# Kernel optimization log

Measured on AMD Instinct MI355X. Metric: run time of the kernel, lower is better.

The kernel has to match this reference:

```python
import jax, jax.numpy as jnp
import numpy as np

WS = 7          # window size
NH = 8          # num heads
EMBED = 512
HD = EMBED // NH


def _rel_pos_index(ws):
    coords = np.stack(np.meshgrid(np.arange(ws), np.arange(ws), indexing='ij'))  # [2,ws,ws]
    flat = coords.reshape(2, -1)                                                 # [2, ws*ws]
    rel = flat[:, :, None] - flat[:, None, :]                                    # [2, L, L]
    rel = rel.transpose(1, 2, 0).astype(np.int32)                                # [L, L, 2]
    rel[..., 0] += ws - 1
    rel[..., 1] += ws - 1
    rel[..., 0] *= 2 * ws - 1
    return rel.sum(-1)                                                           # [L, L]


def setup_inputs() -> dict:
    key = jax.random.key(0)
    ks = jax.random.split(key, 6)
    B, H, W, C = 8, 126, 126, EMBED
    s = 1.0 / np.sqrt(C)
    return {
        'x': jax.random.normal(ks[0], (B, H * W, C), jnp.float32),
        'in_proj_weight': jax.random.normal(ks[1], (3 * C, C), jnp.float32) * s,
        'in_proj_bias': jax.random.normal(ks[2], (3 * C,), jnp.float32) * 0.02,
        'out_proj_weight': jax.random.normal(ks[3], (C, C), jnp.float32) * s,
        'out_proj_bias': jnp.zeros((C,), jnp.float32),
        'rpe_table': jax.random.normal(ks[4], ((2 * WS - 1) ** 2, NH), jnp.float32) * 0.02,
        'rel_index': jnp.asarray(_rel_pos_index(WS)),
        'H': H,
        'W': W,
    }


def _window_permute(x, ws):
    # x: [B, H, W, C] -> [ws*ws, B*qh*qw, C]  (ISA local permute)
    B, H, W, C = x.shape
    qh, qw = H // ws, W // ws
    x = x.reshape(B, qh, ws, qw, ws, C)
    x = jnp.transpose(x, (2, 4, 0, 1, 3, 5))          # ph, pw, B, qh, qw, C
    return x.reshape(ws * ws, B * qh * qw, C)


def _window_unpermute(x, ws, B, H, W):
    qh, qw = H // ws, W // ws
    C = x.shape[-1]
    x = x.reshape(ws, ws, B, qh, qw, C)
    x = jnp.transpose(x, (2, 3, 0, 4, 1, 5))          # B, qh, ph, qw, pw, C
    return x.reshape(B, H, W, C)


def reference(x, in_proj_weight, in_proj_bias, out_proj_weight, out_proj_bias,
              rpe_table, rel_index, H, W):
    B, N, C = x.shape
    xh = x.reshape(B, H, W, C)
    # H, W divisible by window size -> pad/depad are identity
    xp = _window_permute(xh, WS)                       # [L, Bw, C], L = WS*WS
    L, Bw, _ = xp.shape

    qkv = xp @ in_proj_weight.T + in_proj_bias         # [L, Bw, 3C]
    q, k, v = jnp.split(qkv, 3, axis=-1)
    q = q.reshape(L, Bw, NH, HD) * (HD ** -0.5)
    k = k.reshape(L, Bw, NH, HD)
    v = v.reshape(L, Bw, NH, HD)

    scores = jnp.einsum('lbhd,mbhd->bhlm', q, k)       # [Bw, NH, L, L]
    rpe = rpe_table[rel_index]                          # [L, L, NH]
    scores = scores + jnp.transpose(rpe, (2, 0, 1))[None]
    attn = jax.nn.softmax(scores, axis=-1)
    out = jnp.einsum('bhlm,mbhd->lbhd', attn, v).reshape(L, Bw, C)
    out = out @ out_proj_weight.T + out_proj_bias       # [L, Bw, C]

    out = _window_unpermute(out, WS, B, H, W)
    return out.reshape(B, N, C)
```

## Files before the change

### kernel.cpp

```cpp
#include <hip/hip_runtime.h>
#include <hip/hip_bf16.h>
#include <stdint.h>

typedef __attribute__((ext_vector_type(8))) short short8;
typedef __attribute__((ext_vector_type(4))) float f32x4;
typedef __hip_bfloat16 bf16;

#define MFMA16(a, b, c) __builtin_amdgcn_mfma_f32_16x16x32_bf16(a, b, c, 0, 0, 0)

__device__ __forceinline__ uint32_t swz(uint32_t row, uint32_t bir) {
  return bir ^ ((row & 7u) << 4);
}
__device__ __forceinline__ short f2bs(float v) {
  bf16 b = __float2bfloat16(v);
  return *reinterpret_cast<short*>(&b);
}
__device__ __forceinline__ float b2f(bf16 b) { return __bfloat162float(b); }

__device__ __forceinline__ short8 cvt8(f32x4 a, f32x4 b) {
  short8 v;
  v[0] = f2bs(a[0]); v[1] = f2bs(a[1]); v[2] = f2bs(a[2]); v[3] = f2bs(a[3]);
  v[4] = f2bs(b[0]); v[5] = f2bs(b[1]); v[6] = f2bs(b[2]); v[7] = f2bs(b[3]);
  return v;
}

__device__ __forceinline__ void gl_lds16(const void* g, void* l) {
  __builtin_amdgcn_global_load_lds(
      (const __attribute__((address_space(1))) unsigned int*)g,
      (__attribute__((address_space(3))) unsigned int*)l, 16, 0, 0);
}

__global__ __launch_bounds__(256) void k_conv_w4(
    const float* __restrict__ wqkv, const float* __restrict__ bqkv,
    const float* __restrict__ wo,   const float* __restrict__ bo,
    const float* __restrict__ rpe,  const int* __restrict__ relidx,
    char* __restrict__ wqkvb, bf16* __restrict__ bqkvb,
    char* __restrict__ wob,   bf16* __restrict__ bob,
    bf16* __restrict__ rpew)
{
  int b = blockIdx.x, t = threadIdx.x;
  if (b < 384) {
    long i = (long)b * 2048 + t * 8;
    int row = (int)(i >> 9);
    uint32_t g = ((uint32_t)i & 511u) >> 3;
    f32x4 a = *(const f32x4*)(wqkv + i), c = *(const f32x4*)(wqkv + i + 4);
    *reinterpret_cast<short8*>(wqkvb + (size_t)row * 1024 + ((g * 16) ^ ((row & 7u) << 4))) = cvt8(a, c);
  } else if (b < 512) {
    long i = (long)(b - 384) * 2048 + t * 8;
    int row = (int)(i >> 9);
    uint32_t g = ((uint32_t)i & 511u) >> 3;
    f32x4 a = *(const f32x4*)(wo + i), c = *(const f32x4*)(wo + i + 4);
    *reinterpret_cast<short8*>(wob + (size_t)row * 1024 + ((g * 16) ^ ((row & 7u) << 4))) = cvt8(a, c);
  } else if (b == 512) {
    for (int j = t; j < 1536; j += 256) bqkvb[j] = __float2bfloat16(bqkv[j]);
    for (int j = t; j < 512;  j += 256) bob[j]  = __float2bfloat16(bo[j]);
  } else {
    int h = b - 513;
    for (int e = t; e < 3136; e += 256) {
      int q = e >> 6, c = e & 63;
      float v = (c < 49) ? rpe[(long)relidx[q * 49 + c] * 8 + h] : 0.f;
      rpew[h * 3136 + e] = __float2bfloat16(v);
    }
  }
}

__global__ __launch_bounds__(256) void k_conv_x3(
    const float* __restrict__ x, char* __restrict__ xb)
{
  int R  = blockIdx.x * 4 + (threadIdx.x >> 6);
  int c8 = threadIdx.x & 63;
  f32x4 a = {0.f, 0.f, 0.f, 0.f}, b = a;
  if (R < 127008) {
    a = *(const f32x4*)(x + (size_t)R * 512 + c8 * 8);
    b = *(const f32x4*)(x + (size_t)R * 512 + c8 * 8 + 4);
  }
  *reinterpret_cast<short8*>(xb + (size_t)R * 1024 + ((uint32_t)(c8 * 16) ^ ((R & 7u) << 4))) = cvt8(a, b);
}

__global__ __launch_bounds__(256) void k_qkv_gemm6(
    const char* __restrict__ xb,
    const char* __restrict__ wqkvb,
    const bf16* __restrict__ bqkvb,
    char* __restrict__ blob,
    int cb_)
{
  __shared__ __align__(16) char sA[16384];
  __shared__ __align__(16) char sB[16384];

  const int tid = threadIdx.x, lane = tid & 63, w = tid >> 6;
  const int r16 = lane & 15, hi = lane >> 4;

  const int raw = blockIdx.x;
  const int xcd = raw & 7, grp = raw >> 3;
  const int nb = grp % 12, mg = grp / 12;
  const int mtile = mg * 8 + xcd;
  if (mtile >= 249) return;
  const int row0 = cb_ * 31752 + mtile * 128;

  const char* Abase = xb + (size_t)row0 * 1024;
  const char* Bbase = wqkvb + (size_t)nb * 131072;

  const uint32_t rxA = ((uint32_t)((r16 + row0) & 7)) << 4;
  const uint32_t rxB = ((uint32_t)(r16 & 7)) << 4;

  const f32x4 fz = {0.f, 0.f, 0.f, 0.f};
  f32x4 acc[4][4];
  #pragma unroll
  for (int m = 0; m < 4; ++m)
    #pragma unroll
    for (int n = 0; n < 4; ++n) acc[m][n] = fz;

  for (int k0 = 0; k0 < 8; ++k0) {
    if (k0) __syncthreads();
    #pragma unroll
    for (int j = 0; j < 8; ++j) {
      int ch = w * 8 + j;
      if (ch < 16)
        gl_lds16(Abase + (size_t)(ch * 8 + (lane >> 3)) * 1024 + k0 * 128 + (lane & 7) * 16,
                 sA + ch * 1024);
      else {
        int c2 = ch - 16;
        gl_lds16(Bbase + (size_t)(c2 * 8 + (lane >> 3)) * 1024 + k0 * 128 + (lane & 7) * 16,
                 sB + c2 * 1024);
      }
    }
    __syncthreads();

    #pragma unroll
    for (int ks = 0; ks < 2; ++ks) {
      uint32_t cb = (uint32_t)((ks * 4 + hi) * 16);
      short8 aF[4], bF[4];
      #pragma unroll
      for (int m = 0; m < 4; ++m)
        aF[m] = *(const short8*)(sA + ((w & 1) * 64 + m * 16 + r16) * 128 + (cb ^ rxA));
      #pragma unroll
      for (int n = 0; n < 4; ++n)
        bF[n] = *(const short8*)(sB + ((w >> 1) * 64 + n * 16 + r16) * 128 + (cb ^ rxB));
      #pragma unroll
      for (int m = 0; m < 4; ++m)
        #pragma unroll
        for (int n = 0; n < 4; ++n)
          acc[m][n] = MFMA16(aF[m], bF[n], acc[m][n]);
    }
  }

  const int gcol = nb * 128 + (w >> 1) * 64;
  const int t = gcol >> 9;
  const int h = (gcol >> 6) & 7;
  const float scale = (t == 0) ? 0.125f : 1.0f;

  float bias4[4];
  #pragma unroll
  for (int n = 0; n < 4; ++n) bias4[n] = b2f(bqkvb[gcol + n * 16 + r16]);

  #pragma unroll
  for (int m = 0; m < 4; ++m)
    #pragma unroll
    for (int r = 0; r < 4; ++r) {
      int rnat = row0 + (w & 1) * 64 + m * 16 + hi * 4 + r;
      int rem = rnat - cb_ * 31752;
      if (rem >= 31752) continue;
      int b2 = rem / 15876, rem2 = rem - b2 * 15876;
      int y = rem2 / 126, xc = rem2 - y * 126;
      int qi = y / 7, ph = y - qi * 7;
      int qj = xc / 7, pw = xc - qj * 7;
      int wiL = b2 * 324 + qi * 18 + qj, wrow = ph * 7 + pw;
      char* tile = blob + ((size_t)(t * 648 + wiL) * 8 + h) * 8192;
      #pragma unroll
      for (int n = 0; n < 4; ++n) {
        int d = n * 16 + r16;
        bf16 v = __float2bfloat16((acc[m][n][r] + bias4[n]) * scale);
        if (t < 2)
          *(bf16*)(tile + wrow * 128 + ((uint32_t)(2 * d) ^ ((wrow & 7u) << 4))) = v;
        else
          *(bf16*)(tile + wrow * 128 + 2 * d) = v;
      }
    }
}

__global__ __launch_bounds__(256) void k_attn6(
    const char* __restrict__ blob,
    const bf16* __restrict__ rpew,
    char* __restrict__ attnb,
    int cb_)
{
  __shared__ __align__(16) char sQ[8192];
  __shared__ __align__(16) char sK[8192];
  __shared__ __align__(16) char sV[8192];
  __shared__ __align__(16) char sP[8192];

  const int tid = threadIdx.x, lane = tid & 63, w = tid >> 6;
  const int r16 = lane & 15, hi = lane >> 4;
  const int wiL = blockIdx.x >> 3, h = blockIdx.x & 7;

  const char* qb = blob + ((size_t)(0 * 648 + wiL) * 8 + h) * 8192;
  const char* kb = blob + ((size_t)(1 * 648 + wiL) * 8 + h) * 8192;
  const char* vb = blob + ((size_t)(2 * 648 + wiL) * 8 + h) * 8192;

  #pragma unroll
  for (int j = 0; j < 6; ++j) {
    int ch = w * 6 + j;
    int rg = ch >> 3, sub = ch & 7;
    const char* src = (rg == 0 ? qb : rg == 1 ? kb : vb) + sub * 1024 + lane * 16;
    char* dst = (rg == 0 ? sQ : rg == 1 ? sK : sV) + sub * 1024;
    gl_lds16(src, dst);
  }
  __syncthreads();

  const f32x4 fz = {0.f, 0.f, 0.f, 0.f};

  f32x4 s[4];
  #pragma unroll
  for (int n = 0; n < 4; ++n) s[n] = fz;
  #pragma unroll
  for (int k0 = 0; k0 < 2; ++k0) {
    int qrow = w * 16 + r16;
    short8 a = *(const short8*)(sQ + qrow * 128 + swz(qrow, k0 * 64 + hi * 16));
    #pragma unroll
    for (int n = 0; n < 4; ++n) {
      int krow = n * 16 + r16;
      short8 kf = *(const short8*)(sK + krow * 128 + swz(krow, k0 * 64 + hi * 16));
      s[n] = MFMA16(a, kf, s[n]);
    }
  }

  #pragma unroll
  for (int n = 0; n < 4; ++n) {
    int col = n * 16 + r16;
    #pragma unroll
    for (int rr = 0; rr < 4; ++rr) {
      int qrow = w * 16 + hi * 4 + rr;
      int qc = qrow < 49 ? qrow : 48;
      float sv = s[n][rr] + b2f(rpew[h * 3136 + qc * 64 + col]);
      if (col >= 49) sv = -1e30f;
      s[n][rr] = sv;
    }
  }
  #pragma unroll
  for (int rr = 0; rr < 4; ++rr) {
    float mx = fmaxf(fmaxf(s[0][rr], s[1][rr]), fmaxf(s[2][rr], s[3][rr]));
    mx = fmaxf(mx, __shfl_xor(mx, 1));
    mx = fmaxf(mx, __shfl_xor(mx, 2));
    mx = fmaxf(mx, __shfl_xor(mx, 4));
    mx = fmaxf(mx, __shfl_xor(mx, 8));
    float su = 0.f;
    #pragma unroll
    for (int n = 0; n < 4; ++n) {
      float e = __expf(s[n][rr] - mx);
      s[n][rr] = e;
      su += e;
    }
    su += __shfl_xor(su, 1);
    su += __shfl_xor(su, 2);
    su += __shfl_xor(su, 4);
    su += __shfl_xor(su, 8);
    float inv = 1.f / su;
    #pragma unroll
    for (int n = 0; n < 4; ++n) s[n][rr] *= inv;
  }

  char* pw = sP + w * 2048;
  #pragma unroll
  for (int n = 0; n < 4; ++n)
    #pragma unroll
    for (int rr = 0; rr < 4; ++rr) {
      int rl = hi * 4 + rr, col = n * 16 + r16;
      *(bf16*)(pw + rl * 128 + swz(rl, 2 * col)) = __float2bfloat16(s[n][rr]);
    }
  __syncthreads();

  char* sVt = sQ;
  {
    int k = tid >> 2, c0 = (tid & 3) * 16;
    short8 v0 = *(const short8*)(sV + k * 128 + 2 * c0);
    short8 v1 = *(const short8*)(sV + k * 128 + 2 * c0 + 16);
    #pragma unroll
    for (int e = 0; e < 8; ++e) {
      int c = c0 + e;
      *(short*)(sVt + c * 128 + ((uint32_t)(2 * k) ^ ((c & 7u) << 4))) = v0[e];
      int c2 = c0 + 8 + e;
      *(short*)(sVt + c2 * 128 + ((uint32_t)(2 * k) ^ ((c2 & 7u) << 4))) = v1[e];
    }
  }
  __syncthreads();

  f32x4 o[4];
  #pragma unroll
  for (int n = 0; n < 4; ++n) o[n] = fz;
  #pragma unroll
  for (int k0 = 0; k0 < 2; ++k0) {
    short8 a = *(const short8*)(pw + r16 * 128 + swz(r16, k0 * 64 + hi * 16));
    #pragma unroll
    for (int n = 0; n < 4; ++n) {
      int d = n * 16 + r16;
      short8 vf = *(const short8*)(sVt + d * 128 + swz(d, k0 * 64 + hi * 16));
      o[n] = MFMA16(a, vf, o[n]);
    }
  }

  const int b2 = wiL / 324, wr = wiL - b2 * 324;
  const int qi = wr / 18, qj = wr - qi * 18;
  const int rowBase = (cb_ * 2 + b2) * 15876 + qi * 882 + qj * 7;
  #pragma unroll
  for (int n = 0; n < 4; ++n) {
    int d = n * 16 + r16;
    #pragma unroll
    for (int r = 0; r < 4; ++r) {
      int wrow = w * 16 + hi * 4 + r;
      if (wrow < 49) {
        int rnat = rowBase + (wrow / 7) * 126 + wrow % 7;
        *(bf16*)(attnb + (size_t)rnat * 1024 +
                 ((uint32_t)(h * 128 + 2 * d) ^ ((rnat & 7u) << 4))) =
            __float2bfloat16(o[n][r]);
      }
    }
  }
}

__global__ __launch_bounds__(256) void k_out_gemm3(
    const char* __restrict__ attnb,
    const char* __restrict__ wob,
    const bf16* __restrict__ bob,
    float* __restrict__ out)
{
  __shared__ __align__(16) char sA[16384];
  __shared__ __align__(16) char sB[16384];

  const int tid = threadIdx.x, lane = tid & 63, w = tid >> 6;
  const int r16 = lane & 15, hi = lane >> 4;

  const int raw = blockIdx.x;
  const int xcd = raw & 7, grp = raw >> 3;
  const int nb = grp & 3, mg = grp >> 2;
  const int mtile = mg * 8 + xcd;
  if (mtile >= 993) return;
  const int row0 = mtile * 128;

  const char* Abase = attnb + (size_t)row0 * 1024;
  const char* Bbase = wob + (size_t)nb * 131072;

  const f32x4 fz = {0.f, 0.f, 0.f, 0.f};
  f32x4 acc[4][4];
  #pragma unroll
  for (int m = 0; m < 4; ++m)
    #pragma unroll
    for (int n = 0; n < 4; ++n) acc[m][n] = fz;

  for (int k0 = 0; k0 < 8; ++k0) {
    if (k0) __syncthreads();
    #pragma unroll
    for (int j = 0; j < 8; ++j) {
      int ch = w * 8 + j;
      if (ch < 16)
        gl_lds16(Abase + (size_t)(ch * 8 + (lane >> 3)) * 1024 + k0 * 128 + (lane & 7) * 16,
                 sA + ch * 1024);
      else {
        int c2 = ch - 16;
        gl_lds16(Bbase + (size_t)(c2 * 8 + (lane >> 3)) * 1024 + k0 * 128 + (lane & 7) * 16,
                 sB + c2 * 1024);
      }
    }
    __syncthreads();

    #pragma unroll
    for (int ks = 0; ks < 2; ++ks) {
      uint32_t cb = (uint32_t)((ks * 4 + hi) * 16) ^ ((r16 & 7u) << 4);
      short8 aF[4], bF[4];
      #pragma unroll
      for (int m = 0; m < 4; ++m)
        aF[m] = *(const short8*)(sA + ((w & 1) * 64 + m * 16 + r16) * 128 + cb);
      #pragma unroll
      for (int n = 0; n < 4; ++n)
        bF[n] = *(const short8*)(sB + ((w >> 1) * 64 + n * 16 + r16) * 128 + cb);
      #pragma unroll
      for (int m = 0; m < 4; ++m)
        #pragma unroll
        for (int n = 0; n < 4; ++n)
          acc[m][n] = MFMA16(aF[m], bF[n], acc[m][n]);
    }
  }

  #pragma unroll
  for (int n = 0; n < 4; ++n) {
    int col = nb * 128 + (w >> 1) * 64 + n * 16 + r16;
    float bias = b2f(bob[col]);
    #pragma unroll
    for (int m = 0; m < 4; ++m)
      #pragma unroll
      for (int r = 0; r < 4; ++r) {
        int row = row0 + (w & 1) * 64 + m * 16 + hi * 4 + r;
        if (row < 127008)
          out[(size_t)row * 512 + col] = acc[m][n][r] + bias;
      }
  }
}

extern "C" void kernel_launch(void* const* d_in, const int* in_sizes, int n_in,
                              void* d_out, int out_size, void* d_ws, size_t ws_size,
                              hipStream_t stream) {
  const float* x      = (const float*)d_in[0];
  const float* wqkv   = (const float*)d_in[1];
  const float* bqkv   = (const float*)d_in[2];
  const float* wo     = (const float*)d_in[3];
  const float* bo     = (const float*)d_in[4];
  const float* rpe    = (const float*)d_in[5];
  const int*   relidx = (const int*)d_in[6];

  char* ws = (char*)d_ws;
  const size_t OFF_XB    = 256;
  const size_t SZ_XB     = 127232ull * 1024;
  const size_t OFF_ATTNB = OFF_XB + SZ_XB;
  const size_t SZ_ATTNB  = 127104ull * 1024;
  const size_t OFF_BLOB  = OFF_ATTNB + SZ_ATTNB;
  const size_t SZ_BLOB   = 3ull * 648 * 8 * 8192;
  const size_t OFF_WQKV  = OFF_BLOB + SZ_BLOB;
  const size_t OFF_WO    = OFF_WQKV + 1536ull * 1024;
  const size_t OFF_BQKV  = OFF_WO + 512ull * 1024;
  const size_t OFF_BO    = OFF_BQKV + 3072;
  const size_t OFF_RPEW  = OFF_BO + 1024;

  char* xb    = ws + OFF_XB;
  char* attnb = ws + OFF_ATTNB;
  char* blob  = ws + OFF_BLOB;
  char* wqkvb = ws + OFF_WQKV;
  char* wob   = ws + OFF_WO;
  bf16* bqkvb = (bf16*)(ws + OFF_BQKV);
  bf16* bob   = (bf16*)(ws + OFF_BO);
  bf16* rpew  = (bf16*)(ws + OFF_RPEW);

  k_conv_w4<<<dim3(521), dim3(256), 0, stream>>>(wqkv, bqkv, wo, bo, rpe, relidx,
                                                 wqkvb, bqkvb, wob, bob, rpew);
  k_conv_x3<<<dim3(31808), dim3(256), 0, stream>>>(x, xb);
  for (int c = 0; c < 4; ++c) {
    k_qkv_gemm6<<<dim3(3072), dim3(256), 0, stream>>>(xb, wqkvb, bqkvb, blob, c);
    k_attn6<<<dim3(5184), dim3(256), 0, stream>>>(blob, rpew, attnb, c);
  }
  k_out_gemm3<<<dim3(4000), dim3(256), 0, stream>>>(attnb, wob, bob, (float*)d_out);
}
```

Measured before the change: 704.5 us.

## Fuse fp32-to-bf16 conversion of x into the QKV GEMM A-tile load

Removes the standalone x conversion kernel and the bf16 staging buffer. The QKV GEMM now loads fp32 rows of x into registers, prefetches the next K-slice, converts to bf16 and writes swizzled into LDS, while B tiles still use direct global-to-LDS loads. This avoids the extra write and reread of the converted buffer, but each N-block now reads fp32 activations at twice the bytes and converts them redundantly across the 12 column blocks.

```diff
diff --git a/kernel.cpp b/kernel.cpp
--- a/kernel.cpp
+++ b/kernel.cpp
@@ -64,21 +64,8 @@
   }
 }
 
-__global__ __launch_bounds__(256) void k_conv_x3(
-    const float* __restrict__ x, char* __restrict__ xb)
-{
-  int R  = blockIdx.x * 4 + (threadIdx.x >> 6);
-  int c8 = threadIdx.x & 63;
-  f32x4 a = {0.f, 0.f, 0.f, 0.f}, b = a;
-  if (R < 127008) {
-    a = *(const f32x4*)(x + (size_t)R * 512 + c8 * 8);
-    b = *(const f32x4*)(x + (size_t)R * 512 + c8 * 8 + 4);
-  }
-  *reinterpret_cast<short8*>(xb + (size_t)R * 1024 + ((uint32_t)(c8 * 16) ^ ((R & 7u) << 4))) = cvt8(a, b);
-}
-
-__global__ __launch_bounds__(256) void k_qkv_gemm6(
-    const char* __restrict__ xb,
+__global__ __launch_bounds__(256) void k_qkv_gemm7(
+    const float* __restrict__ x,
     const char* __restrict__ wqkvb,
     const bf16* __restrict__ bqkvb,
     char* __restrict__ blob,
@@ -97,11 +84,257 @@
   if (mtile >= 249) return;
   const int row0 = cb_ * 31752 + mtile * 128;
 
-  const char* Abase = xb + (size_t)row0 * 1024;
+  const int lrow  = tid >> 1;
+  const int halfc = tid & 1;
+  const int growc = (row0 + lrow < 127008) ? row0 + lrow : 127007;
+  const float* xrow = x + (size_t)growc * 512 + halfc * 32;
+  char* sArow = sA + lrow * 128;
+  const uint32_t wkey = ((uint32_t)(lrow & 7)) << 4;
+
   const char* Bbase = wqkvb + (size_t)nb * 131072;
-
-  const uint32_t rxA = ((uint32_t)((r16 + row0) & 7)) << 4;
-  const uint32_t rxB = ((uint32_t)(r16 & 7)) << 4;
+  const uint32_t rxL = ((uint32_t)(r16 & 7)) << 4;
+
+  const f32x4 fz = {0.f, 0.f, 0.f, 0.f};
+  f32x4 acc[4][4];
+  #pragma unroll
+  for (int m = 0; m < 4; ++m)
+    #pragma unroll
+    for (int n = 0; n < 4; ++n) acc[m][n] = fz;
+
+  f32x4 pa[8];
+  #pragma unroll
+  for (int j = 0; j < 8; ++j) pa[j] = *(const f32x4*)(xrow + j * 4);
+
+  for (int k0 = 0; k0 < 8; ++k0) {
+    if (k0) __syncthreads();
+    #pragma unroll
+    for (int j = 0; j < 4; ++j)
+      *(short8*)(sArow + (((uint32_t)(halfc * 64 + j * 16)) ^ wkey)) =
+          cvt8(pa[2 * j], pa[2 * j + 1]);
+    #pragma unroll
+    for (int j = 0; j < 4; ++j) {
+      int ch = w * 4 + j;
+      gl_lds16(Bbase + (size_t)(ch * 8 + (lane >> 3)) * 1024 + k0 * 128 + (lane & 7) * 16,
+               sB + ch * 1024);
+    }
+    __syncthreads();
+    if (k0 < 7) {
+      const float* src = xrow + (k0 + 1) * 64;
+      #pragma unroll
+      for (int j = 0; j < 8; ++j) pa[j] = *(const f32x4*)(src + j * 4);
+    }
+    #pragma unroll
+    for (int ks = 0; ks < 2; ++ks) {
+      uint32_t cb = (uint32_t)((ks * 4 + hi) * 16);
+      short8 aF[4], bF[4];
+      #pragma unroll
+      for (int m = 0; m < 4; ++m)
+        aF[m] = *(const short8*)(sA + ((w & 1) * 64 + m * 16 + r16) * 128 + (cb ^ rxL));
+      #pragma unroll
+      for (int n = 0; n < 4; ++n)
+        bF[n] = *(const short8*)(sB + ((w >> 1) * 64 + n * 16 + r16) * 128 + (cb ^ rxL));
+      #pragma unroll
+      for (int m = 0; m < 4; ++m)
+        #pragma unroll
+        for (int n = 0; n < 4; ++n)
+          acc[m][n] = MFMA16(aF[m], bF[n], acc[m][n]);
+    }
+  }
+
+  const int gcol = nb * 128 + (w >> 1) * 64;
+  const int t = gcol >> 9;
+  const int h = (gcol >> 6) & 7;
+  const float scale = (t == 0) ? 0.125f : 1.0f;
+
+  float bias4[4];
+  #pragma unroll
+  for (int n = 0; n < 4; ++n) bias4[n] = b2f(bqkvb[gcol + n * 16 + r16]);
+
+  #pragma unroll
+  for (int m = 0; m < 4; ++m)
+    #pragma unroll
+    for (int r = 0; r < 4; ++r) {
+      int rnat = row0 + (w & 1) * 64 + m * 16 + hi * 4 + r;
+      int rem = rnat - cb_ * 31752;
+      if (rem >= 31752) continue;
+      int b2 = rem / 15876, rem2 = rem - b2 * 15876;
+      int y = rem2 / 126, xc = rem2 - y * 126;
+      int qi = y / 7, ph = y - qi * 7;
+      int qj = xc / 7, pw = xc - qj * 7;
+      int wiL = b2 * 324 + qi * 18 + qj, wrow = ph * 7 + pw;
+      char* tile = blob + ((size_t)(t * 648 + wiL) * 8 + h) * 8192;
+      #pragma unroll
+      for (int n = 0; n < 4; ++n) {
+        int d = n * 16 + r16;
+        bf16 v = __float2bfloat16((acc[m][n][r] + bias4[n]) * scale);
+        if (t < 2)
+          *(bf16*)(tile + wrow * 128 + ((uint32_t)(2 * d) ^ ((wrow & 7u) << 4))) = v;
+        else
+          *(bf16*)(tile + wrow * 128 + 2 * d) = v;
+      }
+    }
+}
+
+__global__ __launch_bounds__(256) void k_attn6(
+    const char* __restrict__ blob,
+    const bf16* __restrict__ rpew,
+    char* __restrict__ attnb,
+    int cb_)
+{
+  __shared__ __align__(16) char sQ[8192];
+  __shared__ __align__(16) char sK[8192];
+  __shared__ __align__(16) char sV[8192];
+  __shared__ __align__(16) char sP[8192];
+
+  const int tid = threadIdx.x, lane = tid & 63, w = tid >> 6;
+  const int r16 = lane & 15, hi = lane >> 4;
+  const int wiL = blockIdx.x >> 3, h = blockIdx.x & 7;
+
+  const char* qb = blob + ((size_t)(0 * 648 + wiL) * 8 + h) * 8192;
+  const char* kb = blob + ((size_t)(1 * 648 + wiL) * 8 + h) * 8192;
+  const char* vb = blob + ((size_t)(2 * 648 + wiL) * 8 + h) * 8192;
+
+  #pragma unroll
+  for (int j = 0; j < 6; ++j) {
+    int ch = w * 6 + j;
+    int rg = ch >> 3, sub = ch & 7;
+    const char* src = (rg == 0 ? qb : rg == 1 ? kb : vb) + sub * 1024 + lane * 16;
+    char* dst = (rg == 0 ? sQ : rg == 1 ? sK : sV) + sub * 1024;
+    gl_lds16(src, dst);
+  }
+  __syncthreads();
+
+  const f32x4 fz = {0.f, 0.f, 0.f, 0.f};
+
+  f32x4 s[4];
+  #pragma unroll
+  for (int n = 0; n < 4; ++n) s[n] = fz;
+  #pragma unroll
+  for (int k0 = 0; k0 < 2; ++k0) {
+    int qrow = w * 16 + r16;
+    short8 a = *(const short8*)(sQ + qrow * 128 + swz(qrow, k0 * 64 + hi * 16));
+    #pragma unroll
+    for (int n = 0; n < 4; ++n) {
+      int krow = n * 16 + r16;
+      short8 kf = *(const short8*)(sK + krow * 128 + swz(krow, k0 * 64 + hi * 16));
+      s[n] = MFMA16(a, kf, s[n]);
+    }
+  }
+
+  #pragma unroll
+  for (int n = 0; n < 4; ++n) {
+    int col = n * 16 + r16;
+    #pragma unroll
+    for (int rr = 0; rr < 4; ++rr) {
+      int qrow = w * 16 + hi * 4 + rr;
+      int qc = qrow < 49 ? qrow : 48;
+      float sv = s[n][rr] + b2f(rpew[h * 3136 + qc * 64 + col]);
+      if (col >= 49) sv = -1e30f;
+      s[n][rr] = sv;
+    }
+  }
+  #pragma unroll
+  for (int rr = 0; rr < 4; ++rr) {
+    float mx = fmaxf(fmaxf(s[0][rr], s[1][rr]), fmaxf(s[2][rr], s[3][rr]));
+    mx = fmaxf(mx, __shfl_xor(mx, 1));
+    mx = fmaxf(mx, __shfl_xor(mx, 2));
+    mx = fmaxf(mx, __shfl_xor(mx, 4));
+    mx = fmaxf(mx, __shfl_xor(mx, 8));
+    float su = 0.f;
+    #pragma unroll
+    for (int n = 0; n < 4; ++n) {
+      float e = __expf(s[n][rr] - mx);
+      s[n][rr] = e;
+      su += e;
+    }
+    su += __shfl_xor(su, 1);
+    su += __shfl_xor(su, 2);
+    su += __shfl_xor(su, 4);
+    su += __shfl_xor(su, 8);
+    float inv = 1.f / su;
+    #pragma unroll
+    for (int n = 0; n < 4; ++n) s[n][rr] *= inv;
+  }
+
+  char* pw = sP + w * 2048;
+  #pragma unroll
+  for (int n = 0; n < 4; ++n)
+    #pragma unroll
+    for (int rr = 0; rr < 4; ++rr) {
+      int rl = hi * 4 + rr, col = n * 16 + r16;
+      *(bf16*)(pw + rl * 128 + swz(rl, 2 * col)) = __float2bfloat16(s[n][rr]);
+    }
+  __syncthreads();
+
+  char* sVt = sQ;
+  {
+    int k = tid >> 2, c0 = (tid & 3) * 16;
+    short8 v0 = *(const short8*)(sV + k * 128 + 2 * c0);
+    short8 v1 = *(const short8*)(sV + k * 128 + 2 * c0 + 16);
+    #pragma unroll
+    for (int e = 0; e < 8; ++e) {
+      int c = c0 + e;
+      *(short*)(sVt + c * 128 + ((uint32_t)(2 * k) ^ ((c & 7u) << 4))) = v0[e];
+      int c2 = c0 + 8 + e;
+      *(short*)(sVt + c2 * 128 + ((uint32_t)(2 * k) ^ ((c2 & 7u) << 4))) = v1[e];
+    }
+  }
+  __syncthreads();
+
+  f32x4 o[4];
+  #pragma unroll
+  for (int n = 0; n < 4; ++n) o[n] = fz;
+  #pragma unroll
+  for (int k0 = 0; k0 < 2; ++k0) {
+    short8 a = *(const short8*)(pw + r16 * 128 + swz(r16, k0 * 64 + hi * 16));
+    #pragma unroll
+    for (int n = 0; n < 4; ++n) {
+      int d = n * 16 + r16;
+      short8 vf = *(const short8*)(sVt + d * 128 + swz(d, k0 * 64 + hi * 16));
+      o[n] = MFMA16(a, vf, o[n]);
+    }
+  }
+
+  const int b2 = wiL / 324, wr = wiL - b2 * 324;
+  const int qi = wr / 18, qj = wr - qi * 18;
+  const int rowBase = (cb_ * 2 + b2) * 15876 + qi * 882 + qj * 7;
+  #pragma unroll
+  for (int n = 0; n < 4; ++n) {
+    int d = n * 16 + r16;
+    #pragma unroll
+    for (int r = 0; r < 4; ++r) {
+      int wrow = w * 16 + hi * 4 + r;
+      if (wrow < 49) {
+        int rnat = rowBase + (wrow / 7) * 126 + wrow % 7;
+        *(bf16*)(attnb + (size_t)rnat * 1024 +
+                 ((uint32_t)(h * 128 + 2 * d) ^ ((rnat & 7u) << 4))) =
+            __float2bfloat16(o[n][r]);
+      }
+    }
+  }
+}
+
+__global__ __launch_bounds__(256) void k_out_gemm3(
+    const char* __restrict__ attnb,
+    const char* __restrict__ wob,
+    const bf16* __restrict__ bob,
+    float* __restrict__ out)
+{
+  __shared__ __align__(16) char sA[16384];
+  __shared__ __align__(16) char sB[16384];
+
+  const int tid = threadIdx.x, lane = tid & 63, w = tid >> 6;
+  const int r16 = lane & 15, hi = lane >> 4;
+
+  const int raw = blockIdx.x;
+  const int xcd = raw & 7, grp = raw >> 3;
+  const int nb = grp & 3, mg = grp >> 2;
+  const int mtile = mg * 8 + xcd;
+  if (mtile >= 993) return;
+  const int row0 = mtile * 128;
+
+  const char* Abase = attnb + (size_t)row0 * 1024;
+  const char* Bbase = wob + (size_t)nb * 131072;
 
   const f32x4 fz = {0.f, 0.f, 0.f, 0.f};
   f32x4 acc[4][4];
@@ -128,242 +361,6 @@
 
     #pragma unroll
     for (int ks = 0; ks < 2; ++ks) {
-      uint32_t cb = (uint32_t)((ks * 4 + hi) * 16);
-      short8 aF[4], bF[4];
-      #pragma unroll
-      for (int m = 0; m < 4; ++m)
-        aF[m] = *(const short8*)(sA + ((w & 1) * 64 + m * 16 + r16) * 128 + (cb ^ rxA));
-      #pragma unroll
-      for (int n = 0; n < 4; ++n)
-        bF[n] = *(const short8*)(sB + ((w >> 1) * 64 + n * 16 + r16) * 128 + (cb ^ rxB));
-      #pragma unroll
-      for (int m = 0; m < 4; ++m)
-        #pragma unroll
-        for (int n = 0; n < 4; ++n)
-          acc[m][n] = MFMA16(aF[m], bF[n], acc[m][n]);
-    }
-  }
-
-  const int gcol = nb * 128 + (w >> 1) * 64;
-  const int t = gcol >> 9;
-  const int h = (gcol >> 6) & 7;
-  const float scale = (t == 0) ? 0.125f : 1.0f;
-
-  float bias4[4];
-  #pragma unroll
-  for (int n = 0; n < 4; ++n) bias4[n] = b2f(bqkvb[gcol + n * 16 + r16]);
-
-  #pragma unroll
-  for (int m = 0; m < 4; ++m)
-    #pragma unroll
-    for (int r = 0; r < 4; ++r) {
-      int rnat = row0 + (w & 1) * 64 + m * 16 + hi * 4 + r;
-      int rem = rnat - cb_ * 31752;
-      if (rem >= 31752) continue;
-      int b2 = rem / 15876, rem2 = rem - b2 * 15876;
-      int y = rem2 / 126, xc = rem2 - y * 126;
-      int qi = y / 7, ph = y - qi * 7;
-      int qj = xc / 7, pw = xc - qj * 7;
-      int wiL = b2 * 324 + qi * 18 + qj, wrow = ph * 7 + pw;
-      char* tile = blob + ((size_t)(t * 648 + wiL) * 8 + h) * 8192;
-      #pragma unroll
-      for (int n = 0; n < 4; ++n) {
-        int d = n * 16 + r16;
-        bf16 v = __float2bfloat16((acc[m][n][r] + bias4[n]) * scale);
-        if (t < 2)
-          *(bf16*)(tile + wrow * 128 + ((uint32_t)(2 * d) ^ ((wrow & 7u) << 4))) = v;
-        else
-          *(bf16*)(tile + wrow * 128 + 2 * d) = v;
-      }
-    }
-}
-
-__global__ __launch_bounds__(256) void k_attn6(
-    const char* __restrict__ blob,
-    const bf16* __restrict__ rpew,
-    char* __restrict__ attnb,
-    int cb_)
-{
-  __shared__ __align__(16) char sQ[8192];
-  __shared__ __align__(16) char sK[8192];
-  __shared__ __align__(16) char sV[8192];
-  __shared__ __align__(16) char sP[8192];
-
-  const int tid = threadIdx.x, lane = tid & 63, w = tid >> 6;
-  const int r16 = lane & 15, hi = lane >> 4;
-  const int wiL = blockIdx.x >> 3, h = blockIdx.x & 7;
-
-  const char* qb = blob + ((size_t)(0 * 648 + wiL) * 8 + h) * 8192;
-  const char* kb = blob + ((size_t)(1 * 648 + wiL) * 8 + h) * 8192;
-  const char* vb = blob + ((size_t)(2 * 648 + wiL) * 8 + h) * 8192;
-
-  #pragma unroll
-  for (int j = 0; j < 6; ++j) {
-    int ch = w * 6 + j;
-    int rg = ch >> 3, sub = ch & 7;
-    const char* src = (rg == 0 ? qb : rg == 1 ? kb : vb) + sub * 1024 + lane * 16;
-    char* dst = (rg == 0 ? sQ : rg == 1 ? sK : sV) + sub * 1024;
-    gl_lds16(src, dst);
-  }
-  __syncthreads();
-
-  const f32x4 fz = {0.f, 0.f, 0.f, 0.f};
-
-  f32x4 s[4];
-  #pragma unroll
-  for (int n = 0; n < 4; ++n) s[n] = fz;
-  #pragma unroll
-  for (int k0 = 0; k0 < 2; ++k0) {
-    int qrow = w * 16 + r16;
-    short8 a = *(const short8*)(sQ + qrow * 128 + swz(qrow, k0 * 64 + hi * 16));
-    #pragma unroll
-    for (int n = 0; n < 4; ++n) {
-      int krow = n * 16 + r16;
-      short8 kf = *(const short8*)(sK + krow * 128 + swz(krow, k0 * 64 + hi * 16));
-      s[n] = MFMA16(a, kf, s[n]);
-    }
-  }
-
-  #pragma unroll
-  for (int n = 0; n < 4; ++n) {
-    int col = n * 16 + r16;
-    #pragma unroll
-    for (int rr = 0; rr < 4; ++rr) {
-      int qrow = w * 16 + hi * 4 + rr;
-      int qc = qrow < 49 ? qrow : 48;
-      float sv = s[n][rr] + b2f(rpew[h * 3136 + qc * 64 + col]);
-      if (col >= 49) sv = -1e30f;
-      s[n][rr] = sv;
-    }
-  }
-  #pragma unroll
-  for (int rr = 0; rr < 4; ++rr) {
-    float mx = fmaxf(fmaxf(s[0][rr], s[1][rr]), fmaxf(s[2][rr], s[3][rr]));
-    mx = fmaxf(mx, __shfl_xor(mx, 1));
-    mx = fmaxf(mx, __shfl_xor(mx, 2));
-    mx = fmaxf(mx, __shfl_xor(mx, 4));
-    mx = fmaxf(mx, __shfl_xor(mx, 8));
-    float su = 0.f;
-    #pragma unroll
-    for (int n = 0; n < 4; ++n) {
-      float e = __expf(s[n][rr] - mx);
-      s[n][rr] = e;
-      su += e;
-    }
-    su += __shfl_xor(su, 1);
-    su += __shfl_xor(su, 2);
-    su += __shfl_xor(su, 4);
-    su += __shfl_xor(su, 8);
-    float inv = 1.f / su;
-    #pragma unroll
-    for (int n = 0; n < 4; ++n) s[n][rr] *= inv;
-  }
-
-  char* pw = sP + w * 2048;
-  #pragma unroll
-  for (int n = 0; n < 4; ++n)
-    #pragma unroll
-    for (int rr = 0; rr < 4; ++rr) {
-      int rl = hi * 4 + rr, col = n * 16 + r16;
-      *(bf16*)(pw + rl * 128 + swz(rl, 2 * col)) = __float2bfloat16(s[n][rr]);
-    }
-  __syncthreads();
-
-  char* sVt = sQ;
-  {
-    int k = tid >> 2, c0 = (tid & 3) * 16;
-    short8 v0 = *(const short8*)(sV + k * 128 + 2 * c0);
-    short8 v1 = *(const short8*)(sV + k * 128 + 2 * c0 + 16);
-    #pragma unroll
-    for (int e = 0; e < 8; ++e) {
-      int c = c0 + e;
-      *(short*)(sVt + c * 128 + ((uint32_t)(2 * k) ^ ((c & 7u) << 4))) = v0[e];
-      int c2 = c0 + 8 + e;
-      *(short*)(sVt + c2 * 128 + ((uint32_t)(2 * k) ^ ((c2 & 7u) << 4))) = v1[e];
-    }
-  }
-  __syncthreads();
-
-  f32x4 o[4];
-  #pragma unroll
-  for (int n = 0; n < 4; ++n) o[n] = fz;
-  #pragma unroll
-  for (int k0 = 0; k0 < 2; ++k0) {
-    short8 a = *(const short8*)(pw + r16 * 128 + swz(r16, k0 * 64 + hi * 16));
-    #pragma unroll
-    for (int n = 0; n < 4; ++n) {
-      int d = n * 16 + r16;
-      short8 vf = *(const short8*)(sVt + d * 128 + swz(d, k0 * 64 + hi * 16));
-      o[n] = MFMA16(a, vf, o[n]);
-    }
-  }
-
-  const int b2 = wiL / 324, wr = wiL - b2 * 324;
-  const int qi = wr / 18, qj = wr - qi * 18;
-  const int rowBase = (cb_ * 2 + b2) * 15876 + qi * 882 + qj * 7;
-  #pragma unroll
-  for (int n = 0; n < 4; ++n) {
-    int d = n * 16 + r16;
-    #pragma unroll
-    for (int r = 0; r < 4; ++r) {
-      int wrow = w * 16 + hi * 4 + r;
-      if (wrow < 49) {
-        int rnat = rowBase + (wrow / 7) * 126 + wrow % 7;
-        *(bf16*)(attnb + (size_t)rnat * 1024 +
-                 ((uint32_t)(h * 128 + 2 * d) ^ ((rnat & 7u) << 4))) =
-            __float2bfloat16(o[n][r]);
-      }
-    }
-  }
-}
-
-__global__ __launch_bounds__(256) void k_out_gemm3(
-    const char* __restrict__ attnb,
-    const char* __restrict__ wob,
-    const bf16* __restrict__ bob,
-    float* __restrict__ out)
-{
-  __shared__ __align__(16) char sA[16384];
-  __shared__ __align__(16) char sB[16384];
-
-  const int tid = threadIdx.x, lane = tid & 63, w = tid >> 6;
-  const int r16 = lane & 15, hi = lane >> 4;
-
-  const int raw = blockIdx.x;
-  const int xcd = raw & 7, grp = raw >> 3;
-  const int nb = grp & 3, mg = grp >> 2;
-  const int mtile = mg * 8 + xcd;
-  if (mtile >= 993) return;
-  const int row0 = mtile * 128;
-
-  const char* Abase = attnb + (size_t)row0 * 1024;
-  const char* Bbase = wob + (size_t)nb * 131072;
-
-  const f32x4 fz = {0.f, 0.f, 0.f, 0.f};
-  f32x4 acc[4][4];
-  #pragma unroll
-  for (int m = 0; m < 4; ++m)
-    #pragma unroll
-    for (int n = 0; n < 4; ++n) acc[m][n] = fz;
-
-  for (int k0 = 0; k0 < 8; ++k0) {
-    if (k0) __syncthreads();
-    #pragma unroll
-    for (int j = 0; j < 8; ++j) {
-      int ch = w * 8 + j;
-      if (ch < 16)
-        gl_lds16(Abase + (size_t)(ch * 8 + (lane >> 3)) * 1024 + k0 * 128 + (lane & 7) * 16,
-                 sA + ch * 1024);
-      else {
-        int c2 = ch - 16;
-        gl_lds16(Bbase + (size_t)(c2 * 8 + (lane >> 3)) * 1024 + k0 * 128 + (lane & 7) * 16,
-                 sB + c2 * 1024);
-      }
-    }
-    __syncthreads();
-
-    #pragma unroll
-    for (int ks = 0; ks < 2; ++ks) {
       uint32_t cb = (uint32_t)((ks * 4 + hi) * 16) ^ ((r16 & 7u) << 4);
       short8 aF[4], bF[4];
       #pragma unroll
@@ -407,9 +404,7 @@
   const int*   relidx = (const int*)d_in[6];
 
   char* ws = (char*)d_ws;
-  const size_t OFF_XB    = 256;
-  const size_t SZ_XB     = 127232ull * 1024;
-  const size_t OFF_ATTNB = OFF_XB + SZ_XB;
+  const size_t OFF_ATTNB = 256;
   const size_t SZ_ATTNB  = 127104ull * 1024;
   const size_t OFF_BLOB  = OFF_ATTNB + SZ_ATTNB;
   const size_t SZ_BLOB   = 3ull * 648 * 8 * 8192;
@@ -419,7 +414,6 @@
   const size_t OFF_BO    = OFF_BQKV + 3072;
   const size_t OFF_RPEW  = OFF_BO + 1024;
 
-  char* xb    = ws + OFF_XB;
   char* attnb = ws + OFF_ATTNB;
   char* blob  = ws + OFF_BLOB;
   char* wqkvb = ws + OFF_WQKV;
@@ -430,9 +424,8 @@
 
   k_conv_w4<<<dim3(521), dim3(256), 0, stream>>>(wqkv, bqkv, wo, bo, rpe, relidx,
                                                  wqkvb, bqkvb, wob, bob, rpew);
-  k_conv_x3<<<dim3(31808), dim3(256), 0, stream>>>(x, xb);
   for (int c = 0; c < 4; ++c) {
-    k_qkv_gemm6<<<dim3(3072), dim3(256), 0, stream>>>(xb, wqkvb, bqkvb, blob, c);
+    k_qkv_gemm7<<<dim3(3072), dim3(256), 0, stream>>>(x, wqkvb, bqkvb, blob, c);
     k_attn6<<<dim3(5184), dim3(256), 0, stream>>>(blob, rpew, attnb, c);
   }
   k_out_gemm3<<<dim3(4000), dim3(256), 0, stream>>>(attnb, wob, bob, (float*)d_out);
```

After: 906.7 us. 1.29x slower.
